# Kernel optimization log

Measured on AMD Instinct MI355X. Metric: run time of the kernel, lower is better.

## Reference

```python
import jax, jax.numpy as jnp
import numpy as np

D_MODEL = 1024
NUM_HEADS = 16
HEAD_DIM = D_MODEL // NUM_HEADS


def setup_inputs() -> dict:
    key = jax.random.key(0)
    ks = jax.random.split(key, 11)
    B, S = 2, 2048
    scale = 1.0 / np.sqrt(D_MODEL)
    inp = {
        "query": jax.random.normal(ks[0], (B, S, D_MODEL), jnp.float32),
        "key": jax.random.normal(ks[1], (B, S, D_MODEL), jnp.float32),
        "value": jax.random.normal(ks[2], (B, S, D_MODEL), jnp.float32),
        "Wq": jax.random.normal(ks[3], (D_MODEL, D_MODEL), jnp.float32) * scale,
        "bq": jnp.zeros((D_MODEL,), jnp.float32),
        "Wk": jax.random.normal(ks[4], (D_MODEL, D_MODEL), jnp.float32) * scale,
        "bk": jnp.zeros((D_MODEL,), jnp.float32),
        "Wv": jax.random.normal(ks[5], (D_MODEL, D_MODEL), jnp.float32) * scale,
        "bv": jnp.zeros((D_MODEL,), jnp.float32),
        "Wo": jax.random.normal(ks[6], (D_MODEL, D_MODEL), jnp.float32) * scale,
        "bo": jnp.zeros((D_MODEL,), jnp.float32),
    }
    return inp


def _split_heads(x):
    # [B, S, D] -> [B, H, S, Dh]
    B, S, _ = x.shape
    return x.reshape(B, S, NUM_HEADS, HEAD_DIM).transpose(0, 2, 1, 3)


def reference(query, key, value, Wq, bq, Wk, bk, Wv, bv, Wo, bo):
    q = _split_heads(query @ Wq.T + bq)   # [B,H,S,Dh]
    k = _split_heads(key @ Wk.T + bk)
    v = _split_heads(value @ Wv.T + bv)
    scores = jnp.einsum('bhqd,bhkd->bhqk', q, k) / jnp.sqrt(
        jnp.asarray(HEAD_DIM, q.dtype))
    probs = jax.nn.softmax(scores, axis=-1)
    ctx = jnp.einsum('bhqk,bhkd->bhqd', probs, v)  # [B,H,S,Dh]
    B, H, S, Dh = ctx.shape
    ctx = ctx.transpose(0, 2, 1, 3).reshape(B, S, H * Dh)  # [B,S,D]
    return ctx @ Wo.T + bo
```

## Files before the change

### kernel.cpp

```cpp
#include <hip/hip_runtime.h>
#include <hip/hip_bf16.h>
#include <stdint.h>

#define D_MODEL 1024
#define NHEADS  16
#define HDIM    64
#define BATCH   2
#define SEQ     2048
#define MROWS   (BATCH*SEQ)

typedef __attribute__((ext_vector_type(8))) short  bf16x8;
typedef __attribute__((ext_vector_type(4))) float  f32x4;
typedef __attribute__((ext_vector_type(4))) int    int4v;

__device__ __forceinline__ unsigned short f2bf(float f) {
  unsigned int u = __float_as_uint(f);
  u = (u + 0x7fffu + ((u >> 16) & 1u)) >> 16;
  return (unsigned short)u;
}

__device__ __forceinline__ unsigned cvtpk_bf16(float lo, float hi) {
  unsigned r;
  asm("v_cvt_pk_bf16_f32 %0, %1, %2" : "=v"(r) : "v"(lo), "v"(hi));
  return r;
}

__device__ __forceinline__ void gload_lds16(const unsigned short* g, unsigned short* l) {
  __builtin_amdgcn_global_load_lds(
      (const __attribute__((address_space(1))) void*)g,
      (__attribute__((address_space(3))) void*)l,
      16, 0, 0);
}

__device__ __forceinline__ int swz_chunk(int row) { return (row + (row >> 3)) & 7; }
__device__ __forceinline__ int swz4(int row) { return (row + (row >> 2)) & 3; }
__device__ __forceinline__ int kperm(int m) {
  return (m & 0x63) | ((m & 0x10) >> 2) | ((m & 0x0C) << 1);
}

struct CvtArgs {
  const float* src[7];
  unsigned short* dst[7];
  int n[7];
};

__global__ __launch_bounds__(256) void cvt_all(CvtArgs a) {
  int t = blockIdx.y;
  const float* s = a.src[t];
  unsigned short* d = a.dst[t];
  int n = a.n[t];
  int stride = gridDim.x * blockDim.x * 4;
  for (int i = (blockIdx.x * blockDim.x + threadIdx.x) * 4; i < n; i += stride) {
    float4 v = *(const float4*)(s + i);
    ushort4 o;
    o.x = f2bf(v.x); o.y = f2bf(v.y); o.z = f2bf(v.z); o.w = f2bf(v.w);
    *(ushort4*)(d + i) = o;
  }
}

__global__ __launch_bounds__(512, 2) void gemm_qkv256(
    const unsigned short* __restrict__ Xq, const unsigned short* __restrict__ Xk,
    const unsigned short* __restrict__ Xv,
    const unsigned short* __restrict__ Wq, const unsigned short* __restrict__ Wk,
    const unsigned short* __restrict__ Wv,
    const float* __restrict__ bq, const float* __restrict__ bk,
    const float* __restrict__ bv,
    unsigned short* __restrict__ oq, unsigned short* __restrict__ ok,
    unsigned short* __restrict__ ov) {
  __shared__ __align__(16) unsigned short LDS[3 * 16384];

  const int tid  = threadIdx.x;
  const int lane = tid & 63;
  const int w8   = tid >> 6;
  const int wr   = w8 >> 2;
  const int wc   = w8 & 3;
  const int g    = lane >> 4;
  const int cl   = lane & 15;

  int fid = blockIdx.x;
  int sid = (fid & 7) * 24 + (fid >> 3);
  int ny = sid / 12, nx = sid % 12;
  int z  = nx >> 2;
  int n0 = (nx & 3) * 256;
  int m0 = ny * 256;

  const unsigned short* X = (z == 0) ? Xq : (z == 1) ? Xk : Xv;
  const unsigned short* W = (z == 0) ? Wq : (z == 1) ? Wk : Wv;
  const float* bias       = (z == 0) ? bq : (z == 1) ? bk : bv;
  float scale = (z == 0) ? 0.18033688011112042f : 1.0f;

  const int srow   = tid >> 2;
  const int schunk = tid & 3;
  const int scol   = (schunk ^ swz4(srow)) * 8;

  auto stageH = [&](int h) {
    if (h >= 64) return;
    int t_ = h >> 1, qa = h & 1;
    unsigned short* buf = LDS + (t_ % 3) * 16384 + qa * 8192;
    const unsigned short* src = qa ? (W + (size_t)(n0 + srow) * D_MODEL)
                                   : (X + (size_t)(m0 + srow) * D_MODEL);
    src += t_ * 32 + scol;
    gload_lds16(src,                          buf + tid * 8);
    gload_lds16(src + (size_t)128 * D_MODEL,  buf + 4096 + tid * 8);
  };

  f32x4 acc[8][4] = {};

  stageH(0); stageH(1); stageH(2); stageH(3);
  asm volatile("s_waitcnt vmcnt(4)" ::: "memory");
  __builtin_amdgcn_s_barrier();
  __builtin_amdgcn_sched_barrier(0);

  for (int t = 0; t < 32; ++t) {
    const unsigned short* Ab = LDS + (t % 3) * 16384;
    const unsigned short* Bb = Ab + 8192;
    bf16x8 af[4], bcache[4];

#pragma unroll
    for (int i = 0; i < 4; ++i) {
      int row = wr * 128 + i * 16 + cl;
      af[i] = *(const bf16x8*)((const char*)Ab + row * 64 + ((g ^ swz4(row)) << 4));
    }
#pragma unroll
    for (int j = 0; j < 4; ++j) {
      int row = wc * 64 + j * 16 + cl;
      bcache[j] = *(const bf16x8*)((const char*)Bb + row * 64 + ((g ^ swz4(row)) << 4));
    }
    stageH(2 * t + 4);
    __builtin_amdgcn_s_barrier();
    __builtin_amdgcn_sched_barrier(0);
    __builtin_amdgcn_s_setprio(1);
#pragma unroll
    for (int i = 0; i < 4; ++i)
#pragma unroll
      for (int j = 0; j < 4; ++j)
        acc[i][j] = __builtin_amdgcn_mfma_f32_16x16x32_bf16(af[i], bcache[j],
                                                            acc[i][j], 0, 0, 0);
    __builtin_amdgcn_s_setprio(0);
    __builtin_amdgcn_s_barrier();
    __builtin_amdgcn_sched_barrier(0);

#pragma unroll
    for (int i = 0; i < 4; ++i) {
      int row = wr * 128 + (4 + i) * 16 + cl;
      af[i] = *(const bf16x8*)((const char*)Ab + row * 64 + ((g ^ swz4(row)) << 4));
    }
    stageH(2 * t + 5);
    __builtin_amdgcn_s_barrier();
    __builtin_amdgcn_sched_barrier(0);
    __builtin_amdgcn_s_setprio(1);
#pragma unroll
    for (int i = 0; i < 4; ++i)
#pragma unroll
      for (int j = 0; j < 4; ++j)
        acc[4 + i][j] = __builtin_amdgcn_mfma_f32_16x16x32_bf16(af[i], bcache[j],
                                                                acc[4 + i][j], 0, 0, 0);
    __builtin_amdgcn_s_setprio(0);
    if (t < 30) {
      asm volatile("s_waitcnt vmcnt(4)" ::: "memory");
    } else if (t == 30) {
      asm volatile("s_waitcnt vmcnt(0)" ::: "memory");
    }
    __builtin_amdgcn_s_barrier();
    __builtin_amdgcn_sched_barrier(0);
  }

  if (z == 2) {
    int b = m0 >> 11;
    int sbase = (m0 & 2047) + wr * 128 + g * 4;
#pragma unroll
    for (int nj = 0; nj < 4; ++nj) {
      int n = n0 + wc * 64 + nj * 16 + cl;
      float bn = bias[n];
      unsigned short* vrow = ov + ((size_t)(b * 1024 + n)) * 2048;
#pragma unroll
      for (int mi = 0; mi < 8; ++mi) {
        int s = sbase + mi * 16;
        uint2 val;
        val.x = cvtpk_bf16(acc[mi][nj][0] + bn, acc[mi][nj][1] + bn);
        val.y = cvtpk_bf16(acc[mi][nj][2] + bn, acc[mi][nj][3] + bn);
        *(uint2*)(vrow + s) = val;
      }
    }
  } else {
    unsigned short* outp = (z == 0) ? oq : ok;
#pragma unroll
    for (int mi = 0; mi < 8; ++mi)
#pragma unroll
      for (int nj = 0; nj < 4; ++nj) {
        int n = n0 + wc * 64 + nj * 16 + cl;
        float bn = bias[n];
        int h = n >> 6, dh = n & 63;
#pragma unroll
        for (int r = 0; r < 4; ++r) {
          int m = m0 + wr * 128 + mi * 16 + g * 4 + r;
          float val = (acc[mi][nj][r] + bn) * scale;
          int b = m >> 11, s = m & 2047;
          outp[(((size_t)(b * NHEADS + h)) * SEQ + s) * HDIM + dh] = f2bf(val);
        }
      }
  }
}

__global__ __launch_bounds__(512) void gemm_out2(
    const unsigned short* __restrict__ Xc, const unsigned short* __restrict__ Wo,
    const float* __restrict__ bo, float* __restrict__ out) {
  __shared__ __align__(16) unsigned short LDS[3 * 8192];

  const int tid  = threadIdx.x;
  const int lane = tid & 63;
  const int w8   = tid >> 6;
  const int wr   = w8 >> 2;
  const int wc   = w8 & 3;
  const int g    = lane >> 4;
  const int cl   = lane & 15;

  int fid = blockIdx.x;
  int sid = (fid & 7) * 32 + (fid >> 3);
  int m0 = (sid >> 3) * 128;
  int n0 = (sid & 7) * 128;

  const int srow   = tid >> 2;
  const int scol   = ((tid & 3) ^ swz4(srow)) * 8;

  auto stage_ = [&](int t_) {
    if (t_ >= 32) return;
    unsigned short* buf = LDS + (t_ % 3) * 8192;
    const unsigned short* sa = Xc + (size_t)(m0 + srow) * D_MODEL + t_ * 32 + scol;
    const unsigned short* sb = Wo + (size_t)(n0 + srow) * D_MODEL + t_ * 32 + scol;
    gload_lds16(sa, buf + tid * 8);
    gload_lds16(sb, buf + 4096 + tid * 8);
  };

  f32x4 acc[4][2] = {};

  stage_(0); stage_(1);
  asm volatile("s_waitcnt vmcnt(2)" ::: "memory");
  __builtin_amdgcn_s_barrier();
  __builtin_amdgcn_sched_barrier(0);

  for (int t = 0; t < 32; ++t) {
    const unsigned short* Ab = LDS + (t % 3) * 8192;
    const unsigned short* Bb = Ab + 4096;
    bf16x8 af[4], bf[2];
#pragma unroll
    for (int i = 0; i < 4; ++i) {
      int row = wr * 64 + i * 16 + cl;
      af[i] = *(const bf16x8*)((const char*)Ab + row * 64 + ((g ^ swz4(row)) << 4));
    }
#pragma unroll
    for (int j = 0; j < 2; ++j) {
      int row = wc * 32 + j * 16 + cl;
      bf[j] = *(const bf16x8*)((const char*)Bb + row * 64 + ((g ^ swz4(row)) << 4));
    }
    stage_(t + 2);
    __builtin_amdgcn_s_barrier();
    __builtin_amdgcn_sched_barrier(0);
    __builtin_amdgcn_s_setprio(1);
#pragma unroll
    for (int i = 0; i < 4; ++i)
#pragma unroll
      for (int j = 0; j < 2; ++j)
        acc[i][j] = __builtin_amdgcn_mfma_f32_16x16x32_bf16(af[i], bf[j],
                                                            acc[i][j], 0, 0, 0);
    __builtin_amdgcn_s_setprio(0);
    if (t < 30) {
      asm volatile("s_waitcnt vmcnt(2)" ::: "memory");
    } else if (t == 30) {
      asm volatile("s_waitcnt vmcnt(0)" ::: "memory");
    }
    __builtin_amdgcn_s_barrier();
    __builtin_amdgcn_sched_barrier(0);
  }

#pragma unroll
  for (int mi = 0; mi < 4; ++mi)
#pragma unroll
    for (int nj = 0; nj < 2; ++nj) {
      int n = n0 + wc * 32 + nj * 16 + cl;
      float bn = bo[n];
#pragma unroll
      for (int r = 0; r < 4; ++r) {
        int m = m0 + wr * 64 + mi * 16 + g * 4 + r;
        out[(size_t)m * D_MODEL + n] = acc[mi][nj][r] + bn;
      }
    }
}

__global__ __launch_bounds__(256, 2) void attn(
    const unsigned short* __restrict__ q, const unsigned short* __restrict__ k,
    const unsigned short* __restrict__ vt, unsigned short* __restrict__ ctx) {
  __shared__ __align__(16) unsigned short K0[128 * 64], V0[64 * 128];
  __shared__ __align__(16) unsigned short K1[128 * 64], V1[64 * 128];

  const int tid  = threadIdx.x;
  const int lane = tid & 63;
  const int wv   = tid >> 6;
  const int g    = lane >> 4;
  const int cl   = lane & 15;

  const int bh = blockIdx.x;
  const int qt = blockIdx.y;

  const unsigned short* qb  = q  + (size_t)bh * SEQ * HDIM;
  const unsigned short* kb  = k  + (size_t)bh * SEQ * HDIM;
  const unsigned short* vbt = vt + (size_t)bh * HDIM * SEQ;

  bf16x8 qf[2][2];
  {
    int qbase = qt * 128 + wv * 32;
#pragma unroll
    for (int qh = 0; qh < 2; ++qh) {
      const unsigned short* qp = qb + (size_t)(qbase + qh * 16 + cl) * HDIM + 8 * g;
      qf[qh][0] = *(const bf16x8*)(qp);
      qf[qh][1] = *(const bf16x8*)(qp + 32);
    }
  }

  const int srowK = tid >> 3;
  const int swzK  = swz_chunk(srowK);
  const int vrow  = tid >> 4;
  const int swzV  = swz_chunk(vrow);
  const int ldst  = tid * 16;

  f32x4 acc0[4] = {}, acc1[4] = {};
  f32x4 accs0 = {}, accs1 = {};
  const int4v onesi = {0x3F803F80, 0x3F803F80, 0x3F803F80, 0x3F803F80};
  const bf16x8 onesb = __builtin_bit_cast(bf16x8, onesi);

  auto stageK_ = [&](int t, unsigned short* Kb) {
    const unsigned short* kt_ = kb + (size_t)t * 128 * HDIM;
#pragma unroll
    for (int c = 0; c < 4; ++c) {
      int row  = srowK + 32 * c;
      int col  = ((tid & 7) ^ swzK ^ ((c & 1) << 2)) * 8;
      gload_lds16(kt_ + (size_t)kperm(row) * HDIM + col,
                  (unsigned short*)((char*)Kb + ldst + c * 4096));
    }
  };
  auto stageV_ = [&](int t, unsigned short* Vb) {
    const unsigned short* vt_ = vbt + t * 128;
#pragma unroll
    for (int c = 0; c < 4; ++c) {
      int row = vrow + 16 * c;
      int sw  = (swzV + 2 * c) & 7;
      int col = (((tid & 7) ^ sw) | (tid & 8)) * 8;
      gload_lds16(vt_ + (size_t)row * SEQ + col,
                  (unsigned short*)((char*)Vb + ldst + c * 4096));
    }
  };

  f32x4 sc[8][2];

  auto qk = [&](const unsigned short* Kb) {
#pragma unroll
    for (int ni = 0; ni < 8; ++ni) { sc[ni][0] = f32x4{}; sc[ni][1] = f32x4{}; }
    __builtin_amdgcn_s_setprio(1);
#pragma unroll
    for (int kc = 0; kc < 2; ++kc)
#pragma unroll
      for (int ni = 0; ni < 8; ++ni) {
        int row  = ni * 16 + cl;
        int byte = row * 128 + (((kc * 4 + g) ^ swz_chunk(row)) << 4);
        bf16x8 kf = *(const bf16x8*)((const char*)Kb + byte);
        sc[ni][0] = __builtin_amdgcn_mfma_f32_16x16x32_bf16(kf, qf[0][kc], sc[ni][0], 0, 0, 0);
        sc[ni][1] = __builtin_amdgcn_mfma_f32_16x16x32_bf16(kf, qf[1][kc], sc[ni][1], 0, 0, 0);
      }
    __builtin_amdgcn_s_setprio(0);
  };

  auto smpack = [&](int4v (&pa0)[4], int4v (&pa1)[4]) {
#pragma unroll
    for (int qh = 0; qh < 2; ++qh)
#pragma unroll
      for (int ni = 0; ni < 8; ++ni)
#pragma unroll
        for (int r = 0; r < 4; ++r)
          sc[ni][qh][r] = __builtin_amdgcn_exp2f(sc[ni][qh][r]);
#pragma unroll
    for (int kcp = 0; kcp < 4; ++kcp) {
      pa0[kcp][0] = (int)cvtpk_bf16(sc[2 * kcp][0][0], sc[2 * kcp][0][1]);
      pa0[kcp][1] = (int)cvtpk_bf16(sc[2 * kcp][0][2], sc[2 * kcp][0][3]);
      pa0[kcp][2] = (int)cvtpk_bf16(sc[2 * kcp + 1][0][0], sc[2 * kcp + 1][0][1]);
      pa0[kcp][3] = (int)cvtpk_bf16(sc[2 * kcp + 1][0][2], sc[2 * kcp + 1][0][3]);
      pa1[kcp][0] = (int)cvtpk_bf16(sc[2 * kcp][1][0], sc[2 * kcp][1][1]);
      pa1[kcp][1] = (int)cvtpk_bf16(sc[2 * kcp][1][2], sc[2 * kcp][1][3]);
      pa1[kcp][2] = (int)cvtpk_bf16(sc[2 * kcp + 1][1][0], sc[2 * kcp + 1][1][1]);
      pa1[kcp][3] = (int)cvtpk_bf16(sc[2 * kcp + 1][1][2], sc[2 * kcp + 1][1][3]);
    }
  };

  auto pv = [&](const unsigned short* Vb, int4v (&pa0)[4], int4v (&pa1)[4]) {
    __builtin_amdgcn_s_setprio(1);
#pragma unroll
    for (int kcp = 0; kcp < 4; ++kcp) {
      bf16x8 a0 = __builtin_bit_cast(bf16x8, pa0[kcp]);
      bf16x8 a1 = __builtin_bit_cast(bf16x8, pa1[kcp]);
#pragma unroll
      for (int nd = 0; nd < 4; ++nd) {
        int row = nd * 16 + cl;
        int c   = kcp * 4 + g;
        int byte = row * 256 + ((((c & 7) ^ swz_chunk(row)) | (c & 8)) << 4);
        bf16x8 vf = *(const bf16x8*)((const char*)Vb + byte);
        acc0[nd] = __builtin_amdgcn_mfma_f32_16x16x32_bf16(a0, vf, acc0[nd], 0, 0, 0);
        acc1[nd] = __builtin_amdgcn_mfma_f32_16x16x32_bf16(a1, vf, acc1[nd], 0, 0, 0);
      }
      accs0 = __builtin_amdgcn_mfma_f32_16x16x32_bf16(a0, onesb, accs0, 0, 0, 0);
      accs1 = __builtin_amdgcn_mfma_f32_16x16x32_bf16(a1, onesb, accs1, 0, 0, 0);
    }
    __builtin_amdgcn_s_setprio(0);
  };

  const int NT = SEQ / 128;
  stageK_(0, K0);
  stageV_(0, V0);
  __syncthreads();
  stageK_(1, K1);
  qk(K0);
  for (int i = 0; i < NT; ++i) {
    int4v pa0[4], pa1[4];
    smpack(pa0, pa1);
    __syncthreads();
    if (i + 2 < NT) stageK_(i + 2, (i & 1) ? K1 : K0);
    if (i + 1 < NT) stageV_(i + 1, (i & 1) ? V0 : V1);
    if (i + 1 < NT) qk((i & 1) ? K0 : K1);
    pv((i & 1) ? V1 : V0, pa0, pa1);
  }

  int b = bh >> 4, h = bh & 15;
#pragma unroll
  for (int r = 0; r < 4; ++r) {
    float i0 = 1.0f / accs0[r];
    float i1 = 1.0f / accs1[r];
#pragma unroll
    for (int qh = 0; qh < 2; ++qh) {
      int srow_o = qt * 128 + wv * 32 + qh * 16 + g * 4 + r;
      float iv = qh ? i1 : i0;
#pragma unroll
      for (int nd = 0; nd < 4; ++nd) {
        int d = nd * 16 + cl;
        float val = (qh ? acc1[nd][r] : acc0[nd][r]) * iv;
        ctx[(((size_t)(b * SEQ + srow_o)) * NHEADS + h) * HDIM + d] = f2bf(val);
      }
    }
  }
}

extern "C" void kernel_launch(void* const* d_in, const int* in_sizes, int n_in,
                              void* d_out, int out_size, void* d_ws, size_t ws_size,
                              hipStream_t stream) {
  (void)in_sizes; (void)n_in; (void)out_size; (void)ws_size;
  const float* query = (const float*)d_in[0];
  const float* key_  = (const float*)d_in[1];
  const float* value = (const float*)d_in[2];
  const float* Wq = (const float*)d_in[3];
  const float* bq = (const float*)d_in[4];
  const float* Wk = (const float*)d_in[5];
  const float* bk = (const float*)d_in[6];
  const float* Wv = (const float*)d_in[7];
  const float* bv = (const float*)d_in[8];
  const float* Wo = (const float*)d_in[9];
  const float* bo = (const float*)d_in[10];
  float* out = (float*)d_out;

  unsigned short* w = (unsigned short*)d_ws;
  const size_t NA = (size_t)MROWS * D_MODEL;
  const size_t NW = (size_t)D_MODEL * D_MODEL;
  unsigned short* Xq  = w;
  unsigned short* Xk  = Xq + NA;
  unsigned short* Xv  = Xk + NA;
  unsigned short* Wqb = Xv + NA;
  unsigned short* Wkb = Wqb + NW;
  unsigned short* Wvb = Wkb + NW;
  unsigned short* Wob = Wvb + NW;
  unsigned short* qs  = Wob + NW;
  unsigned short* ks  = qs + NA;
  unsigned short* vtb = ks + NA;
  unsigned short* cx  = vtb + NA;

  CvtArgs ca;
  ca.src[0] = query; ca.dst[0] = Xq;  ca.n[0] = (int)NA;
  ca.src[1] = key_;  ca.dst[1] = Xk;  ca.n[1] = (int)NA;
  ca.src[2] = value; ca.dst[2] = Xv;  ca.n[2] = (int)NA;
  ca.src[3] = Wq;    ca.dst[3] = Wqb; ca.n[3] = (int)NW;
  ca.src[4] = Wk;    ca.dst[4] = Wkb; ca.n[4] = (int)NW;
  ca.src[5] = Wv;    ca.dst[5] = Wvb; ca.n[5] = (int)NW;
  ca.src[6] = Wo;    ca.dst[6] = Wob; ca.n[6] = (int)NW;

  cvt_all<<<dim3(256, 7, 1), 256, 0, stream>>>(ca);
  gemm_qkv256<<<dim3(192, 1, 1), 512, 0, stream>>>(Xq, Xk, Xv, Wqb, Wkb, Wvb,
                                                   bq, bk, bv, qs, ks, vtb);
  attn<<<dim3(32, 16, 1), 256, 0, stream>>>(qs, ks, vtb, cx);
  gemm_out2<<<dim3(256, 1, 1), 512, 0, stream>>>(cx, Wob, bo, out);
}
```

Before: 116.2 us.

## Fuse fp32-to-bf16 conversion into GEMM loads and drop the separate convert kernel

```diff
diff --git a/kernel.cpp b/kernel.cpp
--- a/kernel.cpp
+++ b/kernel.cpp
@@ -25,6 +25,15 @@
   return r;
 }
 
+__device__ __forceinline__ int4v pack8(const float4& x, const float4& y) {
+  int4v r;
+  r[0] = (int)cvtpk_bf16(x.x, x.y);
+  r[1] = (int)cvtpk_bf16(x.z, x.w);
+  r[2] = (int)cvtpk_bf16(y.x, y.y);
+  r[3] = (int)cvtpk_bf16(y.z, y.w);
+  return r;
+}
+
 __device__ __forceinline__ void gload_lds16(const unsigned short* g, unsigned short* l) {
   __builtin_amdgcn_global_load_lds(
       (const __attribute__((address_space(1))) void*)g,
@@ -38,36 +47,16 @@
   return (m & 0x63) | ((m & 0x10) >> 2) | ((m & 0x0C) << 1);
 }
 
-struct CvtArgs {
-  const float* src[7];
-  unsigned short* dst[7];
-  int n[7];
-};
-
-__global__ __launch_bounds__(256) void cvt_all(CvtArgs a) {
-  int t = blockIdx.y;
-  const float* s = a.src[t];
-  unsigned short* d = a.dst[t];
-  int n = a.n[t];
-  int stride = gridDim.x * blockDim.x * 4;
-  for (int i = (blockIdx.x * blockDim.x + threadIdx.x) * 4; i < n; i += stride) {
-    float4 v = *(const float4*)(s + i);
-    ushort4 o;
-    o.x = f2bf(v.x); o.y = f2bf(v.y); o.z = f2bf(v.z); o.w = f2bf(v.w);
-    *(ushort4*)(d + i) = o;
-  }
-}
-
-__global__ __launch_bounds__(512, 2) void gemm_qkv256(
-    const unsigned short* __restrict__ Xq, const unsigned short* __restrict__ Xk,
-    const unsigned short* __restrict__ Xv,
-    const unsigned short* __restrict__ Wq, const unsigned short* __restrict__ Wk,
-    const unsigned short* __restrict__ Wv,
+__global__ __launch_bounds__(512, 1) void gemm_qkv256(
+    const float* __restrict__ Xq, const float* __restrict__ Xk,
+    const float* __restrict__ Xv,
+    const float* __restrict__ Wq, const float* __restrict__ Wk,
+    const float* __restrict__ Wv,
     const float* __restrict__ bq, const float* __restrict__ bk,
     const float* __restrict__ bv,
     unsigned short* __restrict__ oq, unsigned short* __restrict__ ok,
     unsigned short* __restrict__ ov) {
-  __shared__ __align__(16) unsigned short LDS[3 * 16384];
+  __shared__ __align__(16) unsigned short LDS[2 * 16384];
 
   const int tid  = threadIdx.x;
   const int lane = tid & 63;
@@ -84,85 +73,83 @@
   int n0 = (nx & 3) * 256;
   int m0 = ny * 256;
 
-  const unsigned short* X = (z == 0) ? Xq : (z == 1) ? Xk : Xv;
-  const unsigned short* W = (z == 0) ? Wq : (z == 1) ? Wk : Wv;
-  const float* bias       = (z == 0) ? bq : (z == 1) ? bk : bv;
+  const float* X    = (z == 0) ? Xq : (z == 1) ? Xk : Xv;
+  const float* W    = (z == 0) ? Wq : (z == 1) ? Wk : Wv;
+  const float* bias = (z == 0) ? bq : (z == 1) ? bk : bv;
   float scale = (z == 0) ? 0.18033688011112042f : 1.0f;
 
-  const int srow   = tid >> 2;
-  const int schunk = tid & 3;
-  const int scol   = (schunk ^ swz4(srow)) * 8;
-
-  auto stageH = [&](int h) {
-    if (h >= 64) return;
-    int t_ = h >> 1, qa = h & 1;
-    unsigned short* buf = LDS + (t_ % 3) * 16384 + qa * 8192;
-    const unsigned short* src = qa ? (W + (size_t)(n0 + srow) * D_MODEL)
-                                   : (X + (size_t)(m0 + srow) * D_MODEL);
-    src += t_ * 32 + scol;
-    gload_lds16(src,                          buf + tid * 8);
-    gload_lds16(src + (size_t)128 * D_MODEL,  buf + 4096 + tid * 8);
+  const int sr  = tid >> 1;
+  const int sh  = tid & 1;
+  const int ssw = swz4(sr);
+  const float* Xrow = X + (size_t)(m0 + sr) * D_MODEL + sh * 16;
+  const float* Wrow = W + (size_t)(n0 + sr) * D_MODEL + sh * 16;
+  const int wb0 = sr * 64 + (((2 * sh) ^ ssw) << 4);
+  const int wb1 = sr * 64 + (((2 * sh + 1) ^ ssw) << 4);
+
+  float4 rA[4], rB[4];
+  auto load_t = [&](int t) {
+    const float* pa = Xrow + t * 32;
+    rA[0] = *(const float4*)(pa);     rA[1] = *(const float4*)(pa + 4);
+    rA[2] = *(const float4*)(pa + 8); rA[3] = *(const float4*)(pa + 12);
+    const float* pb = Wrow + t * 32;
+    rB[0] = *(const float4*)(pb);     rB[1] = *(const float4*)(pb + 4);
+    rB[2] = *(const float4*)(pb + 8); rB[3] = *(const float4*)(pb + 12);
+  };
+  auto write_t = [&](int bi) {
+    char* A_ = (char*)(LDS + bi * 16384);
+    char* B_ = A_ + 16384;
+    *(int4v*)(A_ + wb0) = pack8(rA[0], rA[1]);
+    *(int4v*)(A_ + wb1) = pack8(rA[2], rA[3]);
+    *(int4v*)(B_ + wb0) = pack8(rB[0], rB[1]);
+    *(int4v*)(B_ + wb1) = pack8(rB[2], rB[3]);
   };
 
   f32x4 acc[8][4] = {};
 
-  stageH(0); stageH(1); stageH(2); stageH(3);
-  asm volatile("s_waitcnt vmcnt(4)" ::: "memory");
-  __builtin_amdgcn_s_barrier();
-  __builtin_amdgcn_sched_barrier(0);
-
+  load_t(0);
+  write_t(0);
+  __syncthreads();
+
+#pragma unroll 2
   for (int t = 0; t < 32; ++t) {
-    const unsigned short* Ab = LDS + (t % 3) * 16384;
-    const unsigned short* Bb = Ab + 8192;
-    bf16x8 af[4], bcache[4];
-
+    if (t < 31) load_t(t + 1);
+    __builtin_amdgcn_sched_barrier(0);
+    const char* Ab = (const char*)(LDS + (t & 1) * 16384);
+    const char* Bb = Ab + 16384;
+    bf16x8 af[4], bfr[4];
+#pragma unroll
+    for (int j = 0; j < 4; ++j) {
+      int row = wc * 64 + j * 16 + cl;
+      bfr[j] = *(const bf16x8*)(Bb + row * 64 + ((g ^ swz4(row)) << 4));
+    }
 #pragma unroll
     for (int i = 0; i < 4; ++i) {
       int row = wr * 128 + i * 16 + cl;
-      af[i] = *(const bf16x8*)((const char*)Ab + row * 64 + ((g ^ swz4(row)) << 4));
-    }
-#pragma unroll
-    for (int j = 0; j < 4; ++j) {
-      int row = wc * 64 + j * 16 + cl;
-      bcache[j] = *(const bf16x8*)((const char*)Bb + row * 64 + ((g ^ swz4(row)) << 4));
-    }
-    stageH(2 * t + 4);
-    __builtin_amdgcn_s_barrier();
-    __builtin_amdgcn_sched_barrier(0);
+      af[i] = *(const bf16x8*)(Ab + row * 64 + ((g ^ swz4(row)) << 4));
+    }
     __builtin_amdgcn_s_setprio(1);
 #pragma unroll
     for (int i = 0; i < 4; ++i)
 #pragma unroll
       for (int j = 0; j < 4; ++j)
-        acc[i][j] = __builtin_amdgcn_mfma_f32_16x16x32_bf16(af[i], bcache[j],
+        acc[i][j] = __builtin_amdgcn_mfma_f32_16x16x32_bf16(af[i], bfr[j],
                                                             acc[i][j], 0, 0, 0);
     __builtin_amdgcn_s_setprio(0);
-    __builtin_amdgcn_s_barrier();
-    __builtin_amdgcn_sched_barrier(0);
-
 #pragma unroll
     for (int i = 0; i < 4; ++i) {
       int row = wr * 128 + (4 + i) * 16 + cl;
-      af[i] = *(const bf16x8*)((const char*)Ab + row * 64 + ((g ^ swz4(row)) << 4));
-    }
-    stageH(2 * t + 5);
-    __builtin_amdgcn_s_barrier();
-    __builtin_amdgcn_sched_barrier(0);
+      af[i] = *(const bf16x8*)(Ab + row * 64 + ((g ^ swz4(row)) << 4));
+    }
     __builtin_amdgcn_s_setprio(1);
 #pragma unroll
     for (int i = 0; i < 4; ++i)
 #pragma unroll
       for (int j = 0; j < 4; ++j)
-        acc[4 + i][j] = __builtin_amdgcn_mfma_f32_16x16x32_bf16(af[i], bcache[j],
+        acc[4 + i][j] = __builtin_amdgcn_mfma_f32_16x16x32_bf16(af[i], bfr[j],
                                                                 acc[4 + i][j], 0, 0, 0);
     __builtin_amdgcn_s_setprio(0);
-    if (t < 30) {
-      asm volatile("s_waitcnt vmcnt(4)" ::: "memory");
-    } else if (t == 30) {
-      asm volatile("s_waitcnt vmcnt(0)" ::: "memory");
-    }
-    __builtin_amdgcn_s_barrier();
-    __builtin_amdgcn_sched_barrier(0);
+    if (t < 31) write_t((t + 1) & 1);
+    __syncthreads();
   }
 
   if (z == 2) {
@@ -202,10 +189,10 @@
   }
 }
 
-__global__ __launch_bounds__(512) void gemm_out2(
-    const unsigned short* __restrict__ Xc, const unsigned short* __restrict__ Wo,
+__global__ __launch_bounds__(512, 1) void gemm_out2(
+    const unsigned short* __restrict__ Xc, const float* __restrict__ Wo,
     const float* __restrict__ bo, float* __restrict__ out) {
-  __shared__ __align__(16) unsigned short LDS[3 * 8192];
+  __shared__ __align__(16) unsigned short LDS[2 * 8192];
 
   const int tid  = threadIdx.x;
   const int lane = tid & 63;
@@ -220,57 +207,59 @@
   int m0 = (sid >> 3) * 128;
   int n0 = (sid & 7) * 128;
 
-  const int srow   = tid >> 2;
-  const int scol   = ((tid & 3) ^ swz4(srow)) * 8;
-
-  auto stage_ = [&](int t_) {
-    if (t_ >= 32) return;
-    unsigned short* buf = LDS + (t_ % 3) * 8192;
-    const unsigned short* sa = Xc + (size_t)(m0 + srow) * D_MODEL + t_ * 32 + scol;
-    const unsigned short* sb = Wo + (size_t)(n0 + srow) * D_MODEL + t_ * 32 + scol;
-    gload_lds16(sa, buf + tid * 8);
-    gload_lds16(sb, buf + 4096 + tid * 8);
+  const int ar  = tid >> 2;
+  const int as  = tid & 3;
+  const int asw = swz4(ar);
+  const unsigned short* Arow = Xc + (size_t)(m0 + ar) * D_MODEL + (as ^ asw) * 8;
+  const float*          Brow = Wo + (size_t)(n0 + ar) * D_MODEL + (as ^ asw) * 8;
+  const int bwb = ar * 64 + (as << 4);
+
+  float4 rB0, rB1;
+  auto gloadA = [&](int t, int bi) {
+    gload_lds16(Arow + t * 32, LDS + bi * 8192 + tid * 8);
+  };
+  auto loadB = [&](int t) {
+    const float* p = Brow + t * 32;
+    rB0 = *(const float4*)(p);
+    rB1 = *(const float4*)(p + 4);
+  };
+  auto writeB = [&](int bi) {
+    char* B_ = (char*)(LDS + bi * 8192) + 8192;
+    *(int4v*)(B_ + bwb) = pack8(rB0, rB1);
   };
 
   f32x4 acc[4][2] = {};
 
-  stage_(0); stage_(1);
-  asm volatile("s_waitcnt vmcnt(2)" ::: "memory");
-  __builtin_amdgcn_s_barrier();
-  __builtin_amdgcn_sched_barrier(0);
-
+  gloadA(0, 0); loadB(0); writeB(0);
+  __syncthreads();
+
+#pragma unroll 2
   for (int t = 0; t < 32; ++t) {
-    const unsigned short* Ab = LDS + (t % 3) * 8192;
-    const unsigned short* Bb = Ab + 4096;
-    bf16x8 af[4], bf[2];
+    if (t < 31) { gloadA(t + 1, (t + 1) & 1); loadB(t + 1); }
+    __builtin_amdgcn_sched_barrier(0);
+    const char* Ab = (const char*)(LDS + (t & 1) * 8192);
+    const char* Bb = Ab + 8192;
+    bf16x8 af[4], bfr[2];
+#pragma unroll
+    for (int j = 0; j < 2; ++j) {
+      int row = wc * 32 + j * 16 + cl;
+      bfr[j] = *(const bf16x8*)(Bb + row * 64 + ((g ^ swz4(row)) << 4));
+    }
 #pragma unroll
     for (int i = 0; i < 4; ++i) {
       int row = wr * 64 + i * 16 + cl;
-      af[i] = *(const bf16x8*)((const char*)Ab + row * 64 + ((g ^ swz4(row)) << 4));
-    }
-#pragma unroll
-    for (int j = 0; j < 2; ++j) {
-      int row = wc * 32 + j * 16 + cl;
-      bf[j] = *(const bf16x8*)((const char*)Bb + row * 64 + ((g ^ swz4(row)) << 4));
-    }
-    stage_(t + 2);
-    __builtin_amdgcn_s_barrier();
-    __builtin_amdgcn_sched_barrier(0);
+      af[i] = *(const bf16x8*)(Ab + row * 64 + ((g ^ swz4(row)) << 4));
+    }
     __builtin_amdgcn_s_setprio(1);
 #pragma unroll
     for (int i = 0; i < 4; ++i)
 #pragma unroll
       for (int j = 0; j < 2; ++j)
-        acc[i][j] = __builtin_amdgcn_mfma_f32_16x16x32_bf16(af[i], bf[j],
+        acc[i][j] = __builtin_amdgcn_mfma_f32_16x16x32_bf16(af[i], bfr[j],
                                                             acc[i][j], 0, 0, 0);
     __builtin_amdgcn_s_setprio(0);
-    if (t < 30) {
-      asm volatile("s_waitcnt vmcnt(2)" ::: "memory");
-    } else if (t == 30) {
-      asm volatile("s_waitcnt vmcnt(0)" ::: "memory");
-    }
-    __builtin_amdgcn_s_barrier();
-    __builtin_amdgcn_sched_barrier(0);
+    if (t < 31) writeB((t + 1) & 1);
+    __syncthreads();
   }
 
 #pragma unroll
@@ -465,31 +454,13 @@
 
   unsigned short* w = (unsigned short*)d_ws;
   const size_t NA = (size_t)MROWS * D_MODEL;
-  const size_t NW = (size_t)D_MODEL * D_MODEL;
-  unsigned short* Xq  = w;
-  unsigned short* Xk  = Xq + NA;
-  unsigned short* Xv  = Xk + NA;
-  unsigned short* Wqb = Xv + NA;
-  unsigned short* Wkb = Wqb + NW;
-  unsigned short* Wvb = Wkb + NW;
-  unsigned short* Wob = Wvb + NW;
-  unsigned short* qs  = Wob + NW;
+  unsigned short* qs  = w;
   unsigned short* ks  = qs + NA;
   unsigned short* vtb = ks + NA;
   unsigned short* cx  = vtb + NA;
 
-  CvtArgs ca;
-  ca.src[0] = query; ca.dst[0] = Xq;  ca.n[0] = (int)NA;
-  ca.src[1] = key_;  ca.dst[1] = Xk;  ca.n[1] = (int)NA;
-  ca.src[2] = value; ca.dst[2] = Xv;  ca.n[2] = (int)NA;
-  ca.src[3] = Wq;    ca.dst[3] = Wqb; ca.n[3] = (int)NW;
-  ca.src[4] = Wk;    ca.dst[4] = Wkb; ca.n[4] = (int)NW;
-  ca.src[5] = Wv;    ca.dst[5] = Wvb; ca.n[5] = (int)NW;
-  ca.src[6] = Wo;    ca.dst[6] = Wob; ca.n[6] = (int)NW;
-
-  cvt_all<<<dim3(256, 7, 1), 256, 0, stream>>>(ca);
-  gemm_qkv256<<<dim3(192, 1, 1), 512, 0, stream>>>(Xq, Xk, Xv, Wqb, Wkb, Wvb,
+  gemm_qkv256<<<dim3(192, 1, 1), 512, 0, stream>>>(query, key_, value, Wq, Wk, Wv,
                                                    bq, bk, bv, qs, ks, vtb);
   attn<<<dim3(32, 16, 1), 256, 0, stream>>>(qs, ks, vtb, cx);
-  gemm_out2<<<dim3(256, 1, 1), 512, 0, stream>>>(cx, Wob, bo, out);
-}
+  gemm_out2<<<dim3(256, 1, 1), 512, 0, stream>>>(cx, Wo, bo, out);
+}
```

Result: slower. 123.0 us (+5.9%).
